# Kernel tuning notes

Hardware: AMD Instinct MI355X
Metric: run time of the kernel (lower is better)

## Reference

```python
import jax, jax.numpy as jnp
import numpy as np
import math
from itertools import combinations_with_replacement

M_MODES = 10      # photonic modes
N_PHOT = 5        # photons in input state [1,0,1,0,...]
HIDDEN = 100      # number of px phase shifters (hidden_dim)
IN_DIM = 784
N_CLASSES = 10
BATCH = 128

# Fock output states with bunching: multisets of N_PHOT modes -> C(14,5)=2002
_STATES = np.array(list(combinations_with_replacement(range(M_MODES), N_PHOT)), dtype=np.int32)  # [S, n] row indices
_FACT = np.array([
    np.prod([math.factorial(int(c)) for c in np.bincount(s, minlength=M_MODES)])
    for s in _STATES
], dtype=np.float32)  # prod t_j! per output state
# Input-state mode columns (occupied modes) and factorial product (=1 since all occupancies are 1)
_IN_COLS = np.array([0, 2, 4, 6, 8], dtype=np.int32)
# Ryser subsets over n=5 rows
_BITS = np.array([[(k >> i) & 1 for i in range(N_PHOT)] for k in range(2 ** N_PHOT)], dtype=np.float32)  # [K, n]
_SIGNS = ((-1.0) ** (N_PHOT - _BITS.sum(axis=1))).astype(np.float32)  # (-1)^n * (-1)^{|S|}


def _rand_unitary(rng, m):
    z = rng.standard_normal((m, m)) + 1j * rng.standard_normal((m, m))
    q, r = np.linalg.qr(z)
    q = q * (np.diag(r) / np.abs(np.diag(r)))
    return q.astype(np.complex64)


def setup_inputs() -> dict:
    rng = np.random.default_rng(0)
    x = jnp.asarray(rng.standard_normal((BATCH, IN_DIM)), dtype=jnp.float32)
    W1 = jnp.asarray(rng.standard_normal((HIDDEN, IN_DIM)) * 0.03, dtype=jnp.float32)
    b1 = jnp.zeros((HIDDEN,), dtype=jnp.float32)
    UL = _rand_unitary(rng, M_MODES)
    UR = _rand_unitary(rng, M_MODES)
    S = _STATES.shape[0]
    W2 = jnp.asarray(rng.standard_normal((N_CLASSES, S)) * 0.02, dtype=jnp.float32)
    b2 = jnp.zeros((N_CLASSES,), dtype=jnp.float32)
    return {
        "x": x, "W1": W1, "b1": b1,
        "wl_re": jnp.asarray(UL.real), "wl_im": jnp.asarray(UL.imag),
        "wr_re": jnp.asarray(UR.real), "wr_im": jnp.asarray(UR.imag),
        "W2": W2, "b2": b2,
    }


def _forward(x, W1, b1, wl_re, wl_im, wr_re, wr_im, W2, b2):
    B = x.shape[0]
    # downscaling linear + sigmoid -> phase-shifter values px in (0,1)
    h = jax.nn.sigmoid(x @ W1.T + b1)  # [B, HIDDEN]
    # phase shifter i sits on mode i % m; commuting phases on a mode sum
    theta = h.reshape(B, HIDDEN // M_MODES, M_MODES).sum(axis=1)  # [B, m]
    WL = (wl_re + 1j * wl_im).astype(jnp.complex64)
    WR = (wr_re + 1j * wr_im).astype(jnp.complex64)
    phase = jnp.exp(1j * theta.astype(jnp.complex64))  # [B, m]
    # total unitary U = WR @ diag(phase) @ WL
    U = jnp.einsum('pq,bq,qr->bpr', WR, phase, WL)  # [B, m, m]
    A = U[:, :, _IN_COLS]  # columns for occupied input modes -> [B, m, n]
    # per output Fock state, take rows (with multiplicity) -> [B, S, n, n]
    Mx = A[:, jnp.asarray(_STATES), :]
    masks = jnp.asarray(_BITS)   # [K, n]
    signs = jnp.asarray(_SIGNS)  # [K]
    # Ryser: perm = (-1)^n sum_S (-1)^{|S|} prod_j (sum_{i in S} M[i,j])
    rs = jnp.einsum('kn,bsnj->bskj', masks, Mx)       # [B, S, K, n]
    p = jnp.prod(rs, axis=-1)                          # [B, S, K]
    perm = jnp.einsum('k,bsk->bs', signs, p)           # [B, S] complex
    amp = perm / jnp.sqrt(jnp.asarray(_FACT))
    prob = amp.real ** 2 + amp.imag ** 2               # boson-sampling output distribution [B, S]
    return prob @ W2.T + b2                            # output Linear [B, N_CLASSES]


def reference(x, W1, b1, wl_re, wl_im, wr_re, wr_im, W2, b2):
    return _forward(x, W1, b1, wl_re, wl_im, wr_re, wr_im, W2, b2)
```

## Files before the change

### kernel.cpp

```cpp
#include <hip/hip_runtime.h>
#include <utility>
#include <math.h>

#define BATCH     128
#define IN_DIM    784
#define HIDDEN    100
#define MM        10
#define NPH       5
#define NSTATES   2002
#define NCLASSES  10

struct StateTbl { unsigned v[2048]; };
struct RFactTbl { float    v[2048]; };

constexpr StateTbl make_state_tbl() {
    StateTbl t{};
    int idx = 0;
    for (int a = 0; a < MM; ++a)
    for (int b = a; b < MM; ++b)
    for (int c = b; c < MM; ++c)
    for (int d = c; d < MM; ++d)
    for (int e = d; e < MM; ++e) {
        t.v[idx++] = (unsigned)a | ((unsigned)b << 4) | ((unsigned)c << 8) |
                     ((unsigned)d << 12) | ((unsigned)e << 16);
    }
    for (; idx < 2048; ++idx) t.v[idx] = 0;
    return t;
}

constexpr RFactTbl make_rfact_tbl() {
    RFactTbl t{};
    int idx = 0;
    for (int a = 0; a < MM; ++a)
    for (int b = a; b < MM; ++b)
    for (int c = b; c < MM; ++c)
    for (int d = c; d < MM; ++d)
    for (int e = d; e < MM; ++e) {
        int cnt[MM] = {};
        cnt[a]++; cnt[b]++; cnt[c]++; cnt[d]++; cnt[e]++;
        int f = 1;
        for (int m = 0; m < MM; ++m) {
            int kf = 1;
            for (int i = 2; i <= cnt[m]; ++i) kf *= i;
            f *= kf;
        }
        t.v[idx++] = 1.0f / (256.0f * (float)f);
    }
    for (; idx < 2048; ++idx) t.v[idx] = 0.f;
    return t;
}

__device__ const StateTbl STATE_TBL = make_state_tbl();
__device__ const RFactTbl RFACT_TBL = make_rfact_tbl();

template <int K>
__device__ __forceinline__ void glynn_step(
    const float (&mr)[5][5], const float (&mi)[5][5],
    float (&cr)[5], float (&ci)[5], float& accr, float& acci)
{
    constexpr int   bit  = (K & 1) ? 0 : ((K & 2) ? 1 : ((K & 4) ? 2 : 3));
    constexpr int   gray = K ^ (K >> 1);
    constexpr int   row  = bit + 1;
    constexpr float s2   = ((gray >> bit) & 1) ? -2.0f : 2.0f;
    constexpr int   pc   = (gray & 1) + ((gray >> 1) & 1) +
                           ((gray >> 2) & 1) + ((gray >> 3) & 1);
    #pragma unroll
    for (int j = 0; j < 5; ++j) {
        cr[j] = fmaf(s2, mr[row][j], cr[j]);
        ci[j] = fmaf(s2, mi[row][j], ci[j]);
    }
    float pr = cr[0], pi = ci[0];
    #pragma unroll
    for (int j = 1; j < 5; ++j) {
        const float nr = pr * cr[j] - pi * ci[j];
        const float ni = pr * ci[j] + pi * cr[j];
        pr = nr; pi = ni;
    }
    if constexpr ((pc & 1) != 0) { accr -= pr; acci -= pi; }
    else                         { accr += pr; acci += pi; }
}

template <int... Ks>
__device__ __forceinline__ void glynn_run(
    std::integer_sequence<int, Ks...>,
    const float (&mr)[5][5], const float (&mi)[5][5],
    float (&cr)[5], float (&ci)[5], float& accr, float& acci)
{
    (glynn_step<Ks + 1>(mr, mi, cr, ci, accr, acci), ...);
}

__global__ __launch_bounds__(512)
__attribute__((amdgpu_waves_per_eu(2, 2)))
void qc_fused(
    const float* __restrict__ x, const float* __restrict__ W1,
    const float* __restrict__ b1,
    const float* __restrict__ wl_re, const float* __restrict__ wl_im,
    const float* __restrict__ wr_re, const float* __restrict__ wr_im,
    const float* __restrict__ W2, const float* __restrict__ b2,
    float* __restrict__ out)
{
    __shared__ __align__(16) float xs[IN_DIM];
    __shared__ float  part[400];
    __shared__ float  hs[HIDDEN];
    __shared__ float  phc[MM], phs_[MM];
    __shared__ float  plr[50], pli[50];
    __shared__ float2 a2[50];
    __shared__ float  wsum[8][NCLASSES];

    const int b    = blockIdx.x >> 1;
    const int half = blockIdx.x & 1;
    const int tid  = threadIdx.x;

    for (int i = tid; i < IN_DIM; i += 512) xs[i] = x[b * IN_DIM + i];
    __syncthreads();

    if (tid < 400) {
        const int j = tid >> 2, q = tid & 3;
        const float* wrow = W1 + j * IN_DIM + q * 196;
        const float* xr   = xs + q * 196;
        float4 acc = make_float4(0.f, 0.f, 0.f, 0.f);
        #pragma unroll 7
        for (int i = 0; i < 196; i += 4) {
            const float4 w  = *(const float4*)(wrow + i);
            const float4 xv = *(const float4*)(xr + i);
            acc.x += w.x * xv.x; acc.y += w.y * xv.y;
            acc.z += w.z * xv.z; acc.w += w.w * xv.w;
        }
        part[tid] = (acc.x + acc.y) + (acc.z + acc.w);
    }
    __syncthreads();

    if (tid < HIDDEN) {
        const float* p = part + 4 * tid;
        float t = (p[0] + p[1]) + (p[2] + p[3]) + b1[tid];
        hs[tid] = 1.0f / (1.0f + expf(-t));
    }
    __syncthreads();

    if (tid < MM) {
        float th = 0.f;
        #pragma unroll
        for (int g = 0; g < MM; ++g) th += hs[g * MM + tid];
        float sv, cv;
        sincosf(th, &sv, &cv);
        phc[tid] = cv; phs_[tid] = sv;
    }
    __syncthreads();

    if (tid < 50) {
        const int q = tid / 5, c = tid % 5;
        const float lr = wl_re[q * MM + 2 * c], li = wl_im[q * MM + 2 * c];
        plr[tid] = phc[q] * lr - phs_[q] * li;
        pli[tid] = phc[q] * li + phs_[q] * lr;
    }
    __syncthreads();

    if (tid < 50) {
        const int p = tid / 5, c = tid % 5;
        float ar = 0.f, ai = 0.f;
        #pragma unroll
        for (int q = 0; q < MM; ++q) {
            const float rr = wr_re[p * MM + q], ri = wr_im[p * MM + q];
            const float br = plr[q * 5 + c],    bi = pli[q * 5 + c];
            ar += rr * br - ri * bi;
            ai += rr * bi + ri * br;
        }
        a2[tid] = make_float2(ar, ai);
    }
    __syncthreads();

    const int sbase = half * 1001;
    const int send  = sbase + 1001;

    float cls[NCLASSES] = {0,0,0,0,0,0,0,0,0,0};

    #pragma unroll 1
    for (int t = 0; t < 2; ++t) {
        const int s = sbase + (t << 9) + tid;
        if (s < send) {
            const unsigned w = STATE_TBL.v[s];

            float mr[5][5], mi[5][5];
            #pragma unroll
            for (int n = 0; n < 5; ++n) {
                const int base = ((w >> (4 * n)) & 15) * 5;
                #pragma unroll
                for (int j = 0; j < 5; ++j) {
                    const float2 e = a2[base + j];
                    mr[n][j] = e.x; mi[n][j] = e.y;
                }
            }

            float cr[5], ci[5];
            #pragma unroll
            for (int j = 0; j < 5; ++j) {
                cr[j] = ((mr[0][j] + mr[1][j]) + (mr[2][j] + mr[3][j])) + mr[4][j];
                ci[j] = ((mi[0][j] + mi[1][j]) + (mi[2][j] + mi[3][j])) + mi[4][j];
            }
            float accr, acci;
            {
                float pr = cr[0], pi = ci[0];
                #pragma unroll
                for (int j = 1; j < 5; ++j) {
                    const float nr = pr * cr[j] - pi * ci[j];
                    const float ni = pr * ci[j] + pi * cr[j];
                    pr = nr; pi = ni;
                }
                accr = pr; acci = pi;
            }
            glynn_run(std::make_integer_sequence<int, 15>{}, mr, mi,
                      cr, ci, accr, acci);

            const float prob = (accr * accr + acci * acci) * RFACT_TBL.v[s];

            #pragma unroll
            for (int c = 0; c < NCLASSES; ++c)
                cls[c] = fmaf(prob, W2[c * NSTATES + s], cls[c]);
        }
    }

    #pragma unroll
    for (int c = 0; c < NCLASSES; ++c) {
        float v = cls[c];
        #pragma unroll
        for (int off = 32; off > 0; off >>= 1) v += __shfl_down(v, off, 64);
        if ((tid & 63) == 0) wsum[tid >> 6][c] = v;
    }
    __syncthreads();
    if (tid < NCLASSES) {
        float t = 0.f;
        #pragma unroll
        for (int wv = 0; wv < 8; ++wv) t += wsum[wv][tid];
        if (half == 0) t += b2[tid];
        atomicAdd(out + b * NCLASSES + tid, t);
    }
}

extern "C" void kernel_launch(void* const* d_in, const int* in_sizes, int n_in,
                              void* d_out, int out_size, void* d_ws, size_t ws_size,
                              hipStream_t stream)
{
    const float* x     = (const float*)d_in[0];
    const float* W1    = (const float*)d_in[1];
    const float* b1    = (const float*)d_in[2];
    const float* wl_re = (const float*)d_in[3];
    const float* wl_im = (const float*)d_in[4];
    const float* wr_re = (const float*)d_in[5];
    const float* wr_im = (const float*)d_in[6];
    const float* W2    = (const float*)d_in[7];
    const float* b2    = (const float*)d_in[8];
    float*       out   = (float*)d_out;

    qc_fused<<<BATCH * 2, 512, 0, stream>>>(x, W1, b1, wl_re, wl_im,
                                            wr_re, wr_im, W2, b2, out);
}
```

Measured before the change: 82.80 us.

## Split fused kernel into unitary stage and permanent stage with quarter-state blocks

Splits the single fused kernel into two launches. The first computes the per-sample 10x5 matrix once per batch row and writes it to workspace, also seeding the output with the bias. The second uses four blocks per sample, one state per thread, and reduces the W2 projection through shared memory with one wave per class. This stops each half-block from recomputing the W1 GEMV and increases parallelism for the permanent stage. The cost is an extra kernel launch, a global round trip for the intermediate, and more atomics.

```diff
diff --git a/kernel.cpp b/kernel.cpp
--- a/kernel.cpp
+++ b/kernel.cpp
@@ -89,29 +89,25 @@
     (glynn_step<Ks + 1>(mr, mi, cr, ci, accr, acci), ...);
 }
 
-__global__ __launch_bounds__(512)
-__attribute__((amdgpu_waves_per_eu(2, 2)))
-void qc_fused(
+__global__ __launch_bounds__(512) void qc_stageA(
     const float* __restrict__ x, const float* __restrict__ W1,
     const float* __restrict__ b1,
     const float* __restrict__ wl_re, const float* __restrict__ wl_im,
     const float* __restrict__ wr_re, const float* __restrict__ wr_im,
-    const float* __restrict__ W2, const float* __restrict__ b2,
-    float* __restrict__ out)
+    const float* __restrict__ b2,
+    float2* __restrict__ A_ws, float* __restrict__ out)
 {
     __shared__ __align__(16) float xs[IN_DIM];
-    __shared__ float  part[400];
-    __shared__ float  hs[HIDDEN];
-    __shared__ float  phc[MM], phs_[MM];
-    __shared__ float  plr[50], pli[50];
-    __shared__ float2 a2[50];
-    __shared__ float  wsum[8][NCLASSES];
-
-    const int b    = blockIdx.x >> 1;
-    const int half = blockIdx.x & 1;
-    const int tid  = threadIdx.x;
-
-    for (int i = tid; i < IN_DIM; i += 512) xs[i] = x[b * IN_DIM + i];
+    __shared__ float part[400];
+    __shared__ float hs[HIDDEN];
+    __shared__ float phc[MM], phs_[MM];
+    __shared__ float plr[50], pli[50];
+
+    const int b   = blockIdx.x;
+    const int tid = threadIdx.x;
+
+    if (tid < 196) ((float4*)xs)[tid] = ((const float4*)(x + b * IN_DIM))[tid];
+    if (tid < NCLASSES) out[b * NCLASSES + tid] = b2[tid];
     __syncthreads();
 
     if (tid < 400) {
@@ -123,8 +119,8 @@
         for (int i = 0; i < 196; i += 4) {
             const float4 w  = *(const float4*)(wrow + i);
             const float4 xv = *(const float4*)(xr + i);
-            acc.x += w.x * xv.x; acc.y += w.y * xv.y;
-            acc.z += w.z * xv.z; acc.w += w.w * xv.w;
+            acc.x = fmaf(w.x, xv.x, acc.x); acc.y = fmaf(w.y, xv.y, acc.y);
+            acc.z = fmaf(w.z, xv.z, acc.z); acc.w = fmaf(w.w, xv.w, acc.w);
         }
         part[tid] = (acc.x + acc.y) + (acc.z + acc.w);
     }
@@ -132,7 +128,7 @@
 
     if (tid < HIDDEN) {
         const float* p = part + 4 * tid;
-        float t = (p[0] + p[1]) + (p[2] + p[3]) + b1[tid];
+        const float t = (p[0] + p[1]) + (p[2] + p[3]) + b1[tid];
         hs[tid] = 1.0f / (1.0f + expf(-t));
     }
     __syncthreads();
@@ -165,74 +161,81 @@
             ar += rr * br - ri * bi;
             ai += rr * bi + ri * br;
         }
-        a2[tid] = make_float2(ar, ai);
-    }
-    __syncthreads();
-
-    const int sbase = half * 1001;
-    const int send  = sbase + 1001;
-
-    float cls[NCLASSES] = {0,0,0,0,0,0,0,0,0,0};
-
-    #pragma unroll 1
-    for (int t = 0; t < 2; ++t) {
-        const int s = sbase + (t << 9) + tid;
-        if (s < send) {
-            const unsigned w = STATE_TBL.v[s];
-
-            float mr[5][5], mi[5][5];
-            #pragma unroll
-            for (int n = 0; n < 5; ++n) {
-                const int base = ((w >> (4 * n)) & 15) * 5;
-                #pragma unroll
-                for (int j = 0; j < 5; ++j) {
-                    const float2 e = a2[base + j];
-                    mr[n][j] = e.x; mi[n][j] = e.y;
-                }
-            }
-
-            float cr[5], ci[5];
+        A_ws[b * 50 + tid] = make_float2(ar, ai);
+    }
+}
+
+__global__ __launch_bounds__(512)
+__attribute__((amdgpu_waves_per_eu(4, 4)))
+void qc_stageB(
+    const float2* __restrict__ A_ws, const float* __restrict__ W2,
+    float* __restrict__ out)
+{
+    __shared__ float2 a2[50];
+    __shared__ float  probs[512];
+
+    const int tid     = threadIdx.x;
+    const int b       = blockIdx.x >> 2;
+    const int quarter = blockIdx.x & 3;
+    const int sbase   = quarter << 9;
+    const int s       = sbase + tid;
+
+    if (tid < 50) a2[tid] = A_ws[b * 50 + tid];
+    __syncthreads();
+
+    float prob = 0.f;
+    if (s < NSTATES) {
+        const unsigned w = STATE_TBL.v[s];
+
+        float mr[5][5], mi[5][5];
+        #pragma unroll
+        for (int n = 0; n < 5; ++n) {
+            const int base = ((w >> (4 * n)) & 15) * 5;
             #pragma unroll
             for (int j = 0; j < 5; ++j) {
-                cr[j] = ((mr[0][j] + mr[1][j]) + (mr[2][j] + mr[3][j])) + mr[4][j];
-                ci[j] = ((mi[0][j] + mi[1][j]) + (mi[2][j] + mi[3][j])) + mi[4][j];
+                const float2 e = a2[base + j];
+                mr[n][j] = e.x; mi[n][j] = e.y;
             }
-            float accr, acci;
-            {
-                float pr = cr[0], pi = ci[0];
-                #pragma unroll
-                for (int j = 1; j < 5; ++j) {
-                    const float nr = pr * cr[j] - pi * ci[j];
-                    const float ni = pr * ci[j] + pi * cr[j];
-                    pr = nr; pi = ni;
-                }
-                accr = pr; acci = pi;
+        }
+
+        float cr[5], ci[5];
+        #pragma unroll
+        for (int j = 0; j < 5; ++j) {
+            cr[j] = ((mr[0][j] + mr[1][j]) + (mr[2][j] + mr[3][j])) + mr[4][j];
+            ci[j] = ((mi[0][j] + mi[1][j]) + (mi[2][j] + mi[3][j])) + mi[4][j];
+        }
+        float accr, acci;
+        {
+            float pr = cr[0], pi = ci[0];
+            #pragma unroll
+            for (int j = 1; j < 5; ++j) {
+                const float nr = pr * cr[j] - pi * ci[j];
+                const float ni = pr * ci[j] + pi * cr[j];
+                pr = nr; pi = ni;
             }
-            glynn_run(std::make_integer_sequence<int, 15>{}, mr, mi,
-                      cr, ci, accr, acci);
-
-            const float prob = (accr * accr + acci * acci) * RFACT_TBL.v[s];
-
-            #pragma unroll
-            for (int c = 0; c < NCLASSES; ++c)
-                cls[c] = fmaf(prob, W2[c * NSTATES + s], cls[c]);
-        }
-    }
-
-    #pragma unroll
-    for (int c = 0; c < NCLASSES; ++c) {
-        float v = cls[c];
+            accr = pr; acci = pi;
+        }
+        glynn_run(std::make_integer_sequence<int, 15>{}, mr, mi,
+                  cr, ci, accr, acci);
+
+        prob = (accr * accr + acci * acci) * RFACT_TBL.v[s];
+    }
+    probs[tid] = prob;
+    __syncthreads();
+
+    const int wv   = tid >> 6;
+    const int lane = tid & 63;
+    #pragma unroll 1
+    for (int c = wv; c < NCLASSES; c += 8) {
+        const float* w2row = W2 + c * NSTATES + sbase;
+        const int    lim   = (sbase + 512 <= NSTATES) ? 512 : (NSTATES - sbase);
+        float v = 0.f;
+        #pragma unroll
+        for (int k = lane; k < 512; k += 64)
+            if (k < lim) v = fmaf(probs[k], w2row[k], v);
         #pragma unroll
         for (int off = 32; off > 0; off >>= 1) v += __shfl_down(v, off, 64);
-        if ((tid & 63) == 0) wsum[tid >> 6][c] = v;
-    }
-    __syncthreads();
-    if (tid < NCLASSES) {
-        float t = 0.f;
-        #pragma unroll
-        for (int wv = 0; wv < 8; ++wv) t += wsum[wv][tid];
-        if (half == 0) t += b2[tid];
-        atomicAdd(out + b * NCLASSES + tid, t);
+        if (lane == 0) atomicAdd(out + b * NCLASSES + c, v);
     }
 }
 
@@ -250,7 +253,9 @@
     const float* W2    = (const float*)d_in[7];
     const float* b2    = (const float*)d_in[8];
     float*       out   = (float*)d_out;
-
-    qc_fused<<<BATCH * 2, 512, 0, stream>>>(x, W1, b1, wl_re, wl_im,
-                                            wr_re, wr_im, W2, b2, out);
-}
+    float2*      A_ws  = (float2*)d_ws;
+
+    qc_stageA<<<BATCH, 512, 0, stream>>>(x, W1, b1, wl_re, wl_im,
+                                         wr_re, wr_im, b2, A_ws, out);
+    qc_stageB<<<BATCH * 4, 512, 0, stream>>>(A_ws, W2, out);
+}
```

Measured after the change: 83.62 us. No clear change (+1.0%).
